# Optimization experiments

Measured on AMD Instinct MI355X. Metric: run time of the kernel, lower is better.

Reference implementation:

```python
import jax, jax.numpy as jnp
import numpy as np

N = 50000      # nodes
E = 800000     # edges (avg degree 16)
D_IN = 64
H = 128        # capacity
LAT = 64       # latent_dim
LN_EPS = 1e-5


def setup_inputs() -> dict:
    key = jax.random.key(0)
    ks = jax.random.split(key, 16)
    inp = {}
    inp["x"] = jax.random.normal(ks[0], (N, D_IN), dtype=jnp.float32)
    inp["edge_index"] = jax.random.randint(ks[1], (2, E), 0, N)
    dims = [(D_IN, H), (H, H), (H, LAT)]
    ki = 2
    for t in ("m", "v"):  # mu tower / logvar tower
        for i, (di, do) in enumerate(dims):
            s = 1.0 / np.sqrt(di)
            inp[f"{t}Wl{i}"] = jax.random.normal(ks[ki], (do, di), jnp.float32) * s; ki += 1
            inp[f"{t}bl{i}"] = jnp.zeros((do,), jnp.float32)
            inp[f"{t}Wr{i}"] = jax.random.normal(ks[ki], (do, di), jnp.float32) * s; ki += 1
            if i < 2:  # LayerNorm on hidden layers only
                inp[f"{t}g{i}"] = jnp.ones((do,), jnp.float32)
                inp[f"{t}b{i}"] = jnp.zeros((do,), jnp.float32)
    return inp


def _ln(h, g, b):
    m = h.mean(-1, keepdims=True)
    v = h.var(-1, keepdims=True)
    return (h - m) * jax.lax.rsqrt(v + LN_EPS) * g + b


def _sage(h, src, dst, inv_deg, Wl, bl, Wr):
    # mean neighbor aggregation: scatter-add messages h[src] into dst, divide by degree
    agg = jax.ops.segment_sum(h[src], dst, num_segments=N) * inv_deg  # [N, d_in]
    # PyG SAGEConv: lin_l(agg) [with bias] + lin_r(h_root) [no bias]
    return agg @ Wl.T + bl + h @ Wr.T


def _tower(x, src, dst, inv_deg, layers):
    h = x
    L = len(layers)
    for i, lay in enumerate(layers):
        h = _sage(h, src, dst, inv_deg, lay[0], lay[1], lay[2])
        if i < L - 1:
            h = jax.nn.relu(_ln(h, lay[3], lay[4]))
    return h


def reference(x, edge_index,
              mWl0, mbl0, mWr0, mg0, mb0,
              mWl1, mbl1, mWr1, mg1, mb1,
              mWl2, mbl2, mWr2,
              vWl0, vbl0, vWr0, vg0, vb0,
              vWl1, vbl1, vWr1, vg1, vb1,
              vWl2, vbl2, vWr2):
    src, dst = edge_index[0], edge_index[1]
    deg = jax.ops.segment_sum(jnp.ones((E,), x.dtype), dst, num_segments=N)
    inv_deg = (1.0 / jnp.maximum(deg, 1.0))[:, None]
    mu_layers = [(mWl0, mbl0, mWr0, mg0, mb0),
                 (mWl1, mbl1, mWr1, mg1, mb1),
                 (mWl2, mbl2, mWr2)]
    lv_layers = [(vWl0, vbl0, vWr0, vg0, vb0),
                 (vWl1, vbl1, vWr1, vg1, vb1),
                 (vWl2, vbl2, vWr2)]
    mu = _tower(x, src, dst, inv_deg, mu_layers)
    lv = _tower(x, src, dst, inv_deg, lv_layers)
    return mu, lv
```

## Files before the change

### kernel.cpp

```cpp
#include <hip/hip_runtime.h>

#define NN 50000
#define NE 800000
#define MPAD 50048
#define NBK 196
#define FB 98
#define CH4 2048
#define EB4 200000
#define STAGE_CAP 6144

typedef __attribute__((ext_vector_type(8))) short short8;
typedef __attribute__((ext_vector_type(4))) float f32x4;
typedef uint __attribute__((ext_vector_type(4))) uintx4;
typedef uint __attribute__((ext_vector_type(2))) uintx2;

__device__ __forceinline__ ushort f2b(float f) {
    uint u = __builtin_bit_cast(uint, f);
    uint r = (u + 0x7fffu + ((u >> 16) & 1u)) >> 16;
    return (ushort)r;
}
__device__ __forceinline__ uint pk2(float a, float b) {
    return (uint)f2b(a) | ((uint)f2b(b) << 16);
}
__device__ __forceinline__ float blo(uint u) { return __builtin_bit_cast(float, u << 16); }
__device__ __forceinline__ float bhi(uint u) { return __builtin_bit_cast(float, u & 0xffff0000u); }

__device__ __forceinline__ uint enc8u(float y) {
    uint b = __builtin_bit_cast(uint, y * 0x1p-120f) + (1u << 19);
    return (b >> 20) & 0x7fu;
}
__device__ __forceinline__ uint enc8s(float y) {
    uint sb = __builtin_bit_cast(uint, y) & 0x80000000u;
    uint b = __builtin_bit_cast(uint, fabsf(y) * 0x1p-120f) + (1u << 19);
    return ((b >> 20) & 0x7fu) | (sb >> 24);
}

__device__ __forceinline__ void acc8(float* a, uintx4 u) {
    a[0] += blo(u[0]); a[1] += bhi(u[0]);
    a[2] += blo(u[1]); a[3] += bhi(u[1]);
    a[4] += blo(u[2]); a[5] += bhi(u[2]);
    a[6] += blo(u[3]); a[7] += bhi(u[3]);
}
__device__ __forceinline__ void acc4(float* a, uintx2 u) {
    a[0] += blo(u[0]); a[1] += bhi(u[0]);
    a[2] += blo(u[1]); a[3] += bhi(u[1]);
}
template <bool SIGNED>
__device__ __forceinline__ void accf8(float* a, uintx2 u, float c120) {
#pragma unroll
    for (int w = 0; w < 2; ++w) {
        uint v = u[w];
#pragma unroll
        for (int j = 0; j < 4; ++j) {
            uint b = (v >> (8 * j)) & 0xffu;
            uint f = SIGNED ? (((b & 0x80u) << 24) | ((b & 0x7fu) << 20)) : (b << 20);
            a[w * 4 + j] += __builtin_bit_cast(float, f) * c120;
        }
    }
}


struct W2Args {
    const float* srcA[8];
    const float* srcB[8];
    ushort* dst[8];
};


struct PrepArgs {
    const float* x; ushort* xb;
    W2Args w;
    const int* edst; int* bhist;
};

__global__ __launch_bounds__(256) void k_prep(PrepArgs a) {
    __shared__ int h[NBK];
    int b = blockIdx.x;
    int t = threadIdx.x;
    if (b < FB) {
        for (int i = t; i < NBK; i += 256) h[i] = 0;
        __syncthreads();
        int i1 = min((b + 1) * CH4, EB4);
        for (int i = b * CH4 + t; i < i1; i += 256) {
            int4 d = ((const int4*)a.edst)[i];
            atomicAdd(&h[d.x >> 8], 1);
            atomicAdd(&h[d.y >> 8], 1);
            atomicAdd(&h[d.z >> 8], 1);
            atomicAdd(&h[d.w >> 8], 1);
        }
        __syncthreads();
        for (int i = t; i < NBK; i += 256) a.bhist[b * NBK + i] = h[i];
    } else if (b < FB + 512) {
        const int offT[8]   = {0, 16384, 49152, 57344, 65536, 81920, 114688, 122880};
        const int splitT[8] = {64, 128, 128, 0, 64, 128, 128, 0};
        const int logKKT[8] = {7, 8, 7, 7, 7, 8, 7, 7};
        const int ntT[8]    = {8, 8, 4, 4, 8, 8, 4, 4};
        int idx = (b - FB) * 256 + t;
        if (idx >= 131072) return;
        int L = 0;
#pragma unroll
        for (int i = 1; i < 8; ++i) if (idx >= offT[i]) L = i;
        int j = idx - offT[L];
        int lk = logKKT[L];
        int KK = 1 << lk;
        int n = j >> lk;
        int c = j & (KK - 1);
        int split = splitT[L];
        float v = (c < split) ? a.w.srcA[L][n * split + c]
                              : a.w.srcB[L][n * (KK - split) + (c - split)];
        int ks = c >> 5, kseg = (c >> 3) & 3, jj = c & 7;
        int nt = n >> 4, r15 = n & 15;
        int lane = (kseg << 4) | r15;
        int foff = ((ks * ntT[L] + nt) << 9) + (lane << 3) + jj;
        a.w.dst[L][foff] = f2b(v);
    } else {
        int i = (b - FB - 512) * 256 + t;
        if (i < NN * 32) {
            float2 v = *(const float2*)(a.x + (size_t)i * 2);
            *(uint*)(a.xb + (size_t)i * 2) = pk2(v.x, v.y);
        }
    }
}


__global__ __launch_bounds__(256) void k_fscan(const int* __restrict__ bhist,
                                               int* __restrict__ pairRel,
                                               int* __restrict__ bbase) {
    __shared__ int tot[256];
    int b = threadIdx.x;
    int run = 0;
    if (b < NBK) {
        for (int blk = 0; blk < FB; ++blk) {
            int v = bhist[blk * NBK + b];
            pairRel[blk * NBK + b] = run;
            run += v;
        }
    }
    tot[b] = (b < NBK) ? run : 0;
    __syncthreads();
    for (int off = 1; off < 256; off <<= 1) {
        int t = (b >= off) ? tot[b - off] : 0;
        __syncthreads();
        tot[b] += t;
        __syncthreads();
    }
    if (b < NBK) bbase[b] = tot[b] - run;
    if (b == NBK - 1) bbase[NBK] = tot[b];
}

__global__ __launch_bounds__(256) void k_f2(const int* __restrict__ src, const int* __restrict__ dst,
                                            const int* __restrict__ pairRel,
                                            const int* __restrict__ bbase, int2* __restrict__ pairs) {
    __shared__ int cur[NBK];
    for (int i = threadIdx.x; i < NBK; i += 256)
        cur[i] = bbase[i] + pairRel[blockIdx.x * NBK + i];
    __syncthreads();
    int i1 = min((int)(blockIdx.x + 1) * CH4, EB4);
    for (int i = blockIdx.x * CH4 + threadIdx.x; i < i1; i += 256) {
        int4 s = ((const int4*)src)[i];
        int4 d = ((const int4*)dst)[i];
        int p0 = atomicAdd(&cur[d.x >> 8], 1);
        int p1 = atomicAdd(&cur[d.y >> 8], 1);
        int p2 = atomicAdd(&cur[d.z >> 8], 1);
        int p3 = atomicAdd(&cur[d.w >> 8], 1);
        pairs[p0] = (int2){s.x, d.x};
        pairs[p1] = (int2){s.y, d.y};
        pairs[p2] = (int2){s.z, d.z};
        pairs[p3] = (int2){s.w, d.w};
    }
}

__global__ __launch_bounds__(256) void k_f3(const int2* __restrict__ pairs,
                                            const int* __restrict__ bbase,
                                            int* __restrict__ row_start,
                                            float* __restrict__ inv_deg,
                                            int* __restrict__ col) {
    __shared__ int ndeg[256];
    __shared__ int noff[256];
    __shared__ int stage[STAGE_CAP];
    int b = blockIdx.x;
    int base = bbase[b], end = bbase[b + 1];
    int nbase = b << 8;
    int t = threadIdx.x;
    ndeg[t] = 0;
    __syncthreads();
    for (int p = base + t; p < end; p += 256) atomicAdd(&ndeg[pairs[p].y - nbase], 1);
    __syncthreads();
    int d = ndeg[t];
    noff[t] = d;
    __syncthreads();
    for (int off = 1; off < 256; off <<= 1) {
        int v = (t >= off) ? noff[t - off] : 0;
        __syncthreads();
        noff[t] += v;
        __syncthreads();
    }
    int excl = noff[t] - d;
    int node = nbase + t;
    if (node < NN) {
        row_start[node] = base + excl;
        inv_deg[node] = 1.0f / (float)(d > 1 ? d : 1);
    }
    if (b == 0 && t == 0) row_start[NN] = NE;
    __syncthreads();
    noff[t] = excl;
    __syncthreads();
    int cnt = end - base;
    for (int p = base + t; p < end; p += 256) {
        int2 pr = pairs[p];
        int pos = atomicAdd(&noff[pr.y - nbase], 1);
        if (pos < STAGE_CAP) stage[pos] = pr.x;
        else col[base + pos] = pr.x;
    }
    __syncthreads();
    int lim = cnt < STAGE_CAP ? cnt : STAGE_CAP;
    for (int i = t; i < lim; i += 256) col[base + i] = stage[i];
}


__global__ __launch_bounds__(256) void k_agg64(
    const ushort* __restrict__ h,
    const int* __restrict__ row_start, const int* __restrict__ col,
    const float* __restrict__ inv_deg, ushort* __restrict__ o) {
    int gid = blockIdx.x * 256 + threadIdx.x;
    int node = gid >> 4;
    int li = gid & 15;
    if (node >= NN) return;
    int s = row_start[node], e = row_start[node + 1];
    float sc = inv_deg[node];
    const ushort* hb = h + li * 4;
    float a[4] = {0, 0, 0, 0};
    int p = s;
    for (; p + 7 < e; p += 8) {
        int cc[8];
#pragma unroll
        for (int j = 0; j < 8; ++j) cc[j] = __builtin_nontemporal_load(col + p + j);
#pragma unroll
        for (int j = 0; j < 8; ++j) acc4(a, *(const uintx2*)(hb + (size_t)cc[j] * 64));
    }
    for (; p < e; ++p) acc4(a, *(const uintx2*)(hb + (size_t)col[p] * 64));
    uintx2 r;
    r[0] = pk2(a[0] * sc, a[1] * sc);
    r[1] = pk2(a[2] * sc, a[3] * sc);
    *(uintx2*)(o + (size_t)node * 64 + li * 4) = r;
}


template <int D, bool SIGNED>
__global__ __launch_bounds__(256) void k_agg8(
    const uchar* __restrict__ h,
    const int* __restrict__ row_start, const int* __restrict__ col,
    const float* __restrict__ inv_deg, ushort* __restrict__ o) {
    constexpr int LPN = D / 8;
    int gid = blockIdx.x * 256 + threadIdx.x;
    int node = gid / LPN;
    int li = gid & (LPN - 1);
    if (node >= NN) return;
    int s = row_start[node], e = row_start[node + 1];
    float sc = inv_deg[node];
    const uchar* hb = h + li * 8;
    const float c120 = 0x1p120f;
    float a[8] = {0, 0, 0, 0, 0, 0, 0, 0};
    int p = s;
    for (; p + 7 < e; p += 8) {
        int cc[8];
#pragma unroll
        for (int j = 0; j < 8; ++j) cc[j] = __builtin_nontemporal_load(col + p + j);
#pragma unroll
        for (int j = 0; j < 8; ++j) accf8<SIGNED>(a, *(const uintx2*)(hb + (size_t)cc[j] * D), c120);
    }
    for (; p < e; ++p) accf8<SIGNED>(a, *(const uintx2*)(hb + (size_t)col[p] * D), c120);
    uintx4 r;
    r[0] = pk2(a[0] * sc, a[1] * sc);
    r[1] = pk2(a[2] * sc, a[3] * sc);
    r[2] = pk2(a[4] * sc, a[5] * sc);
    r[3] = pk2(a[6] * sc, a[7] * sc);
    *(uintx4*)(o + (size_t)node * D + li * 8) = r;
}


struct GArgs {
    const ushort *A1, *A2, *Wm, *Wv;
    const float *blm, *blv, *gm, *gv, *bbm, *bbv;
    void* out;
    uchar* out8;
};

template <int KH, int NOUT, bool DO_LN, bool DUAL, int ASTR, int AOFFM, int OSTR, int OOFFM, bool F8OUT>
__global__ __launch_bounds__(256, 2) void k_gemm(GArgs a) {
    constexpr int NT = NOUT / 16;
    constexpr int NK = KH / 16;
    constexpr int TW = DUAL ? 2 : 1;
    constexpr int WCH = NOUT * KH * 4 / 16;
    __shared__ uint4 wlds[TW * WCH];

    int tid = threadIdx.x;
    int lane = tid & 63, wid = tid >> 6;
    int tow = DUAL ? 0 : blockIdx.y;
    int aoff = tow * AOFFM;

    {
        const uint4* w0 = (const uint4*)(tow ? a.Wv : a.Wm);
        for (int i = tid; i < WCH; i += 256) wlds[i] = w0[i];
        if (DUAL) {
            const uint4* w1 = (const uint4*)a.Wv;
            for (int i = tid; i < WCH; i += 256) wlds[WCH + i] = w1[i];
        }
    }

    int r15 = lane & 15, kseg = lane >> 4;
    int m0 = blockIdx.x * 128 + wid * 32;
    size_t ar0 = (size_t)(m0 + r15);
    size_t ar1 = (size_t)(m0 + 16 + r15);

    short8 af[2][NK];
#pragma unroll
    for (int ks = 0; ks < NK; ++ks) {
        int kc = ks * 32 + kseg * 8;
        af[0][ks] = (kc < KH) ? *(const short8*)(a.A1 + ar0 * ASTR + aoff + kc)
                              : *(const short8*)(a.A2 + ar0 * ASTR + aoff + (kc - KH));
        af[1][ks] = (kc < KH) ? *(const short8*)(a.A1 + ar1 * ASTR + aoff + kc)
                              : *(const short8*)(a.A2 + ar1 * ASTR + aoff + (kc - KH));
    }
    __syncthreads();

    f32x4 acc[TW][2][NT];
#pragma unroll
    for (int tt = 0; tt < TW; ++tt)
#pragma unroll
        for (int t = 0; t < 2; ++t)
#pragma unroll
            for (int nt = 0; nt < NT; ++nt) acc[tt][t][nt] = (f32x4){0.f, 0.f, 0.f, 0.f};

#pragma unroll
    for (int ks = 0; ks < NK; ++ks) {
#pragma unroll
        for (int nt = 0; nt < NT; ++nt) {
#pragma unroll
            for (int tt = 0; tt < TW; ++tt) {
                short8 w = *(const short8*)&wlds[tt * WCH + (ks * NT + nt) * 64 + lane];
                acc[tt][0][nt] = __builtin_amdgcn_mfma_f32_16x16x32_bf16(af[0][ks], w, acc[tt][0][nt], 0, 0, 0);
                acc[tt][1][nt] = __builtin_amdgcn_mfma_f32_16x16x32_bf16(af[1][ks], w, acc[tt][1][nt], 0, 0, 0);
            }
        }
    }

#pragma unroll
    for (int tt = 0; tt < TW; ++tt) {
        int tsel = DUAL ? tt : tow;
        int ooff = tsel * OOFFM;
        const float* bl = tsel ? a.blv : a.blm;
#pragma unroll
        for (int nt = 0; nt < NT; ++nt) {
            float bb = bl[nt * 16 + r15];
#pragma unroll
            for (int t = 0; t < 2; ++t)
#pragma unroll
                for (int r = 0; r < 4; ++r) acc[tt][t][nt][r] += bb;
        }
        if (DO_LN) {
            const float* g = tsel ? a.gv : a.gm;
            const float* b = tsel ? a.bbv : a.bbm;
#pragma unroll
            for (int t = 0; t < 2; ++t) {
                float s[4] = {0, 0, 0, 0}, q[4] = {0, 0, 0, 0};
#pragma unroll
                for (int nt = 0; nt < NT; ++nt)
#pragma unroll
                    for (int r = 0; r < 4; ++r) { float v = acc[tt][t][nt][r]; s[r] += v; q[r] += v * v; }
#pragma unroll
                for (int off = 1; off < 16; off <<= 1)
#pragma unroll
                    for (int r = 0; r < 4; ++r) { s[r] += __shfl_xor(s[r], off); q[r] += __shfl_xor(q[r], off); }
                float mean[4], rstd[4];
#pragma unroll
                for (int r = 0; r < 4; ++r) {
                    mean[r] = s[r] * (1.0f / NOUT);
                    float var = q[r] * (1.0f / NOUT) - mean[r] * mean[r];
                    rstd[r] = rsqrtf(var + 1e-5f);
                }
                ushort* out = (ushort*)a.out;
#pragma unroll
                for (int nt = 0; nt < NT; ++nt) {
                    int n = nt * 16 + r15;
                    float gg = g[n], bb = b[n];
#pragma unroll
                    for (int r = 0; r < 4; ++r) {
                        int row = m0 + t * 16 + kseg * 4 + r;
                        if (row < NN) {
                            float y = fmaxf((acc[tt][t][nt][r] - mean[r]) * rstd[r] * gg + bb, 0.0f);
                            out[(size_t)row * OSTR + ooff + n] = f2b(y);
                            if (F8OUT) a.out8[(size_t)row * OSTR + ooff + n] = (uchar)enc8u(y);
                        }
                    }
                }
            }
        } else {
            float* out = (float*)a.out;
#pragma unroll
            for (int t = 0; t < 2; ++t)
#pragma unroll
                for (int nt = 0; nt < NT; ++nt) {
                    int n = nt * 16 + r15;
#pragma unroll
                    for (int r = 0; r < 4; ++r) {
                        int row = m0 + t * 16 + kseg * 4 + r;
                        if (row < NN) out[(size_t)row * OSTR + ooff + n] = acc[tt][t][nt][r];
                    }
                }
        }
    }
}


struct G2Args {
    const ushort *A, *Wm, *Wv, *a2;
    const float *blm, *blv;
    void *outm, *outv;
};

template <bool FINAL>
__global__ __launch_bounds__(256, 2) void k_gemm2(G2Args a) {
    constexpr int NT = 4, NK = 4;
    constexpr int WCH = 1024;
    __shared__ uint4 wlds[WCH];

    int tid = threadIdx.x;
    int lane = tid & 63, wid = tid >> 6;
    int tow = blockIdx.y;
    {
        const uint4* w0 = (const uint4*)(tow ? a.Wv : a.Wm);
        for (int i = tid; i < WCH; i += 256) wlds[i] = w0[i];
    }
    int r15 = lane & 15, kseg = lane >> 4;
    int m0 = blockIdx.x * 128 + wid * 32;
    size_t ar0 = (size_t)(m0 + r15);
    size_t ar1 = (size_t)(m0 + 16 + r15);
    int aoff = tow * 128;

    short8 af[2][NK];
#pragma unroll
    for (int ks = 0; ks < NK; ++ks) {
        int kc = ks * 32 + kseg * 8;
        af[0][ks] = *(const short8*)(a.A + ar0 * 256 + aoff + kc);
        af[1][ks] = *(const short8*)(a.A + ar1 * 256 + aoff + kc);
    }
    __syncthreads();

    f32x4 acc[2][NT];
#pragma unroll
    for (int t = 0; t < 2; ++t)
#pragma unroll
        for (int nt = 0; nt < NT; ++nt) acc[t][nt] = (f32x4){0.f, 0.f, 0.f, 0.f};

#pragma unroll
    for (int ks = 0; ks < NK; ++ks) {
#pragma unroll
        for (int nt = 0; nt < NT; ++nt) {
            short8 w = *(const short8*)&wlds[(ks * NT + nt) * 64 + lane];
            acc[0][nt] = __builtin_amdgcn_mfma_f32_16x16x32_bf16(af[0][ks], w, acc[0][nt], 0, 0, 0);
            acc[1][nt] = __builtin_amdgcn_mfma_f32_16x16x32_bf16(af[1][ks], w, acc[1][nt], 0, 0, 0);
        }
    }

    if (FINAL) {
        const float* bl = tow ? a.blv : a.blm;
        float* out = (float*)(tow ? a.outv : a.outm);
#pragma unroll
        for (int t = 0; t < 2; ++t)
#pragma unroll
            for (int nt = 0; nt < NT; ++nt) {
                int n = nt * 16 + r15;
                float bb = bl[n];
#pragma unroll
                for (int r = 0; r < 4; ++r) {
                    int row = m0 + t * 16 + kseg * 4 + r;
                    if (row < NN) {
                        float av = blo((uint)a.a2[(size_t)row * 128 + tow * 64 + n]);
                        out[(size_t)row * 64 + n] = acc[t][nt][r] + bb + av;
                    }
                }
            }
    } else {
        uchar* out = (uchar*)a.outm;
#pragma unroll
        for (int t = 0; t < 2; ++t)
#pragma unroll
            for (int nt = 0; nt < NT; ++nt) {
                int n = nt * 16 + r15;
#pragma unroll
                for (int r = 0; r < 4; ++r) {
                    int row = m0 + t * 16 + kseg * 4 + r;
                    if (row < NN) out[(size_t)row * 128 + tow * 64 + n] = (uchar)enc8s(acc[t][nt][r]);
                }
            }
    }
}


extern "C" void kernel_launch(void* const* d_in, const int* in_sizes, int n_in,
                              void* d_out, int out_size, void* d_ws, size_t ws_size,
                              hipStream_t stream) {
    const float* x = (const float*)d_in[0];
    const int* ei = (const int*)d_in[1];
    const int* esrc = ei;
    const int* edst = ei + NE;

    const float* mWl0 = (const float*)d_in[2];
    const float* mbl0 = (const float*)d_in[3];
    const float* mWr0 = (const float*)d_in[4];
    const float* mg0  = (const float*)d_in[5];
    const float* mb0  = (const float*)d_in[6];
    const float* mWl1 = (const float*)d_in[7];
    const float* mbl1 = (const float*)d_in[8];
    const float* mWr1 = (const float*)d_in[9];
    const float* mg1  = (const float*)d_in[10];
    const float* mb1  = (const float*)d_in[11];
    const float* mWl2 = (const float*)d_in[12];
    const float* mbl2 = (const float*)d_in[13];
    const float* mWr2 = (const float*)d_in[14];
    const float* vWl0 = (const float*)d_in[15];
    const float* vbl0 = (const float*)d_in[16];
    const float* vWr0 = (const float*)d_in[17];
    const float* vg0  = (const float*)d_in[18];
    const float* vb0  = (const float*)d_in[19];
    const float* vWl1 = (const float*)d_in[20];
    const float* vbl1 = (const float*)d_in[21];
    const float* vWr1 = (const float*)d_in[22];
    const float* vg1  = (const float*)d_in[23];
    const float* vb1  = (const float*)d_in[24];
    const float* vWl2 = (const float*)d_in[25];
    const float* vbl2 = (const float*)d_in[26];
    const float* vWr2 = (const float*)d_in[27];

    char* p = (char*)d_ws;
    auto alloc = [&](size_t bytes) {
        void* r = (void*)p;
        p += (bytes + 255) & ~(size_t)255;
        return r;
    };
    int* bhist     = (int*)alloc((size_t)FB * NBK * 4);
    int* pairRel   = (int*)alloc((size_t)FB * NBK * 4);
    int* bbase     = (int*)alloc((size_t)(NBK + 1) * 4);
    int* row_start = (int*)alloc((size_t)(NN + 1) * 4);
    float* inv_deg = (float*)alloc((size_t)NN * 4);
    int* col       = (int*)alloc((size_t)NE * 4);
    int2* pairs    = (int2*)alloc((size_t)NE * 8);
    ushort* agg0   = (ushort*)pairs;
    ushort* x_bf   = (ushort*)alloc((size_t)MPAD * 64 * 2);
    ushort* h1p    = (ushort*)alloc((size_t)MPAD * 256 * 2);
    ushort* h2p    = (ushort*)alloc((size_t)MPAD * 256 * 2);
    ushort* aggp   = (ushort*)alloc((size_t)MPAD * 256 * 2);
    uchar* h1f8    = (uchar*)h2p;
    uchar* p2f8    = (uchar*)aggp;
    ushort* a2     = aggp + (size_t)MPAD * 128;
    ushort* wc0    = (ushort*)alloc((size_t)128 * 128 * 2);
    ushort* wc1    = (ushort*)alloc((size_t)128 * 256 * 2);
    ushort* wc2    = (ushort*)alloc((size_t)64 * 128 * 2);
    ushort* wc3    = (ushort*)alloc((size_t)128 * 128 * 2);
    ushort* wc4    = (ushort*)alloc((size_t)128 * 256 * 2);
    ushort* wc5    = (ushort*)alloc((size_t)64 * 128 * 2);
    ushort* wc6    = (ushort*)alloc((size_t)64 * 128 * 2);
    ushort* wc7    = (ushort*)alloc((size_t)64 * 128 * 2);

    float* out_mu = (float*)d_out;
    float* out_lv = (float*)d_out + (size_t)NN * 64;

    PrepArgs pa;
    pa.x = x; pa.xb = x_bf; pa.edst = edst; pa.bhist = bhist;
    pa.w.srcA[0] = mWl0; pa.w.srcB[0] = mWr0; pa.w.dst[0] = wc0;
    pa.w.srcA[1] = mWl1; pa.w.srcB[1] = mWr1; pa.w.dst[1] = wc1;
    pa.w.srcA[2] = mWl2; pa.w.srcB[2] = nullptr; pa.w.dst[2] = wc2;
    pa.w.srcA[3] = nullptr; pa.w.srcB[3] = mWr2; pa.w.dst[3] = wc6;
    pa.w.srcA[4] = vWl0; pa.w.srcB[4] = vWr0; pa.w.dst[4] = wc3;
    pa.w.srcA[5] = vWl1; pa.w.srcB[5] = vWr1; pa.w.dst[5] = wc4;
    pa.w.srcA[6] = vWl2; pa.w.srcB[6] = nullptr; pa.w.dst[6] = wc5;
    pa.w.srcA[7] = nullptr; pa.w.srcB[7] = vWr2; pa.w.dst[7] = wc7;
    k_prep<<<FB + 512 + (NN * 32 + 255) / 256, 256, 0, stream>>>(pa);

    k_fscan<<<1, 256, 0, stream>>>(bhist, pairRel, bbase);
    k_f2<<<FB, 256, 0, stream>>>(esrc, edst, pairRel, bbase, pairs);
    k_f3<<<NBK, 256, 0, stream>>>(pairs, bbase, row_start, inv_deg, col);

    const int gM = MPAD / 128;

    k_agg64<<<(NN * 16 + 255) / 256, 256, 0, stream>>>(x_bf, row_start, col, inv_deg, agg0);
    {
        GArgs ga = {agg0, x_bf, wc0, wc3, mbl0, vbl0, mg0, vg0, mb0, vb0, h1p, h1f8};
        k_gemm<64, 128, true, true, 64, 0, 256, 128, true><<<dim3(gM, 1), 256, 0, stream>>>(ga);
    }
    k_agg8<256, false><<<(NN * 32 + 255) / 256, 256, 0, stream>>>(h1f8, row_start, col, inv_deg, aggp);
    {
        GArgs ga = {aggp, h1p, wc1, wc4, mbl1, vbl1, mg1, vg1, mb1, vb1, h2p, nullptr};
        k_gemm<128, 128, true, false, 256, 128, 256, 128, false><<<dim3(gM, 2), 256, 0, stream>>>(ga);
    }
    {
        G2Args g2 = {h2p, wc2, wc5, nullptr, nullptr, nullptr, p2f8, nullptr};
        k_gemm2<false><<<dim3(gM, 2), 256, 0, stream>>>(g2);
    }
    k_agg8<128, true><<<(NN * 16 + 255) / 256, 256, 0, stream>>>(p2f8, row_start, col, inv_deg, a2);
    {
        G2Args g2 = {h2p, wc6, wc7, a2, mbl2, vbl2, out_mu, out_lv};
        k_gemm2<true><<<dim3(gM, 2), 256, 0, stream>>>(g2);
    }
}
```

Before: 352.6 us.

## Double-buffer weight staging in k_gemm and make row tile configurable

```diff
diff --git a/kernel.cpp b/kernel.cpp
--- a/kernel.cpp
+++ b/kernel.cpp
@@ -35,12 +35,6 @@
     return ((b >> 20) & 0x7fu) | (sb >> 24);
 }
 
-__device__ __forceinline__ void acc8(float* a, uintx4 u) {
-    a[0] += blo(u[0]); a[1] += bhi(u[0]);
-    a[2] += blo(u[1]); a[3] += bhi(u[1]);
-    a[4] += blo(u[2]); a[5] += bhi(u[2]);
-    a[6] += blo(u[3]); a[7] += bhi(u[3]);
-}
 __device__ __forceinline__ void acc4(float* a, uintx2 u) {
     a[0] += blo(u[0]); a[1] += bhi(u[0]);
     a[2] += blo(u[1]); a[3] += bhi(u[1]);
@@ -286,63 +280,83 @@
     uchar* out8;
 };
 
-template <int KH, int NOUT, bool DO_LN, bool DUAL, int ASTR, int AOFFM, int OSTR, int OOFFM, bool F8OUT>
-__global__ __launch_bounds__(256, 2) void k_gemm(GArgs a) {
+template <int KH, int NOUT, bool DO_LN, bool DUAL, int ASTR, int AOFFM, int OSTR, int OOFFM, bool F8OUT, int RT>
+__global__ __launch_bounds__(256, 3) void k_gemm(GArgs a) {
     constexpr int NT = NOUT / 16;
     constexpr int NK = KH / 16;
     constexpr int TW = DUAL ? 2 : 1;
-    constexpr int WCH = NOUT * KH * 4 / 16;
-    __shared__ uint4 wlds[TW * WCH];
+    constexpr int KSB = (TW * NT >= 16) ? 1 : (16 / (TW * NT));
+    constexpr int NC = NK / KSB;
+    constexpr int TCH = KSB * NT * 64;
+    constexpr int CPT = TW * TCH;
+    __shared__ uint4 wlds[2][CPT];
 
     int tid = threadIdx.x;
     int lane = tid & 63, wid = tid >> 6;
     int tow = DUAL ? 0 : blockIdx.y;
     int aoff = tow * AOFFM;
-
-    {
-        const uint4* w0 = (const uint4*)(tow ? a.Wv : a.Wm);
-        for (int i = tid; i < WCH; i += 256) wlds[i] = w0[i];
+    const uint4* w0g = (const uint4*)(tow ? a.Wv : a.Wm);
+    const uint4* w1g = (const uint4*)a.Wv;
+
+    int r15 = lane & 15, kseg = lane >> 4;
+    int m0 = blockIdx.x * (64 * RT) + wid * (16 * RT);
+    size_t ar[RT];
+#pragma unroll
+    for (int t = 0; t < RT; ++t) ar[t] = (size_t)(m0 + t * 16 + r15);
+
+    short8 af[2][RT][KSB];
+
+    auto stageW = [&](int c, int b) {
+        const uint4* p0 = w0g + (size_t)c * TCH;
+#pragma unroll
+        for (int i = 0; i < TCH / 256; ++i) wlds[b][i * 256 + tid] = p0[i * 256 + tid];
         if (DUAL) {
-            const uint4* w1 = (const uint4*)a.Wv;
-            for (int i = tid; i < WCH; i += 256) wlds[WCH + i] = w1[i];
-        }
-    }
-
-    int r15 = lane & 15, kseg = lane >> 4;
-    int m0 = blockIdx.x * 128 + wid * 32;
-    size_t ar0 = (size_t)(m0 + r15);
-    size_t ar1 = (size_t)(m0 + 16 + r15);
-
-    short8 af[2][NK];
-#pragma unroll
-    for (int ks = 0; ks < NK; ++ks) {
-        int kc = ks * 32 + kseg * 8;
-        af[0][ks] = (kc < KH) ? *(const short8*)(a.A1 + ar0 * ASTR + aoff + kc)
-                              : *(const short8*)(a.A2 + ar0 * ASTR + aoff + (kc - KH));
-        af[1][ks] = (kc < KH) ? *(const short8*)(a.A1 + ar1 * ASTR + aoff + kc)
-                              : *(const short8*)(a.A2 + ar1 * ASTR + aoff + (kc - KH));
-    }
-    __syncthreads();
-
-    f32x4 acc[TW][2][NT];
+            const uint4* p1 = w1g + (size_t)c * TCH;
+#pragma unroll
+            for (int i = 0; i < TCH / 256; ++i) wlds[b][TCH + i * 256 + tid] = p1[i * 256 + tid];
+        }
+    };
+    auto loadA = [&](int c, int b) {
+#pragma unroll
+        for (int ko = 0; ko < KSB; ++ko) {
+            int kc = (c * KSB + ko) * 32 + kseg * 8;
+#pragma unroll
+            for (int t = 0; t < RT; ++t)
+                af[b][t][ko] = (kc < KH) ? *(const short8*)(a.A1 + ar[t] * ASTR + aoff + kc)
+                                         : *(const short8*)(a.A2 + ar[t] * ASTR + aoff + (kc - KH));
+        }
+    };
+
+    loadA(0, 0);
+    stageW(0, 0);
+    __syncthreads();
+
+    f32x4 acc[TW][RT][NT];
 #pragma unroll
     for (int tt = 0; tt < TW; ++tt)
 #pragma unroll
-        for (int t = 0; t < 2; ++t)
+        for (int t = 0; t < RT; ++t)
 #pragma unroll
             for (int nt = 0; nt < NT; ++nt) acc[tt][t][nt] = (f32x4){0.f, 0.f, 0.f, 0.f};
 
 #pragma unroll
-    for (int ks = 0; ks < NK; ++ks) {
-#pragma unroll
-        for (int nt = 0; nt < NT; ++nt) {
-#pragma unroll
-            for (int tt = 0; tt < TW; ++tt) {
-                short8 w = *(const short8*)&wlds[tt * WCH + (ks * NT + nt) * 64 + lane];
-                acc[tt][0][nt] = __builtin_amdgcn_mfma_f32_16x16x32_bf16(af[0][ks], w, acc[tt][0][nt], 0, 0, 0);
-                acc[tt][1][nt] = __builtin_amdgcn_mfma_f32_16x16x32_bf16(af[1][ks], w, acc[tt][1][nt], 0, 0, 0);
+    for (int c = 0; c < NC; ++c) {
+        int b = c & 1;
+        if (c + 1 < NC) { stageW(c + 1, b ^ 1); loadA(c + 1, b ^ 1); }
+#pragma unroll
+        for (int ko = 0; ko < KSB; ++ko) {
+#pragma unroll
+            for (int nt = 0; nt < NT; ++nt) {
+#pragma unroll
+                for (int tt = 0; tt < TW; ++tt) {
+                    short8 w = *(const short8*)&wlds[b][tt * TCH + (ko * NT + nt) * 64 + lane];
+#pragma unroll
+                    for (int t = 0; t < RT; ++t)
+                        acc[tt][t][nt] = __builtin_amdgcn_mfma_f32_16x16x32_bf16(af[b][t][ko], w, acc[tt][t][nt], 0, 0, 0);
+                }
             }
         }
+        __syncthreads();
     }
 
 #pragma unroll
@@ -354,15 +368,15 @@
         for (int nt = 0; nt < NT; ++nt) {
             float bb = bl[nt * 16 + r15];
 #pragma unroll
-            for (int t = 0; t < 2; ++t)
+            for (int t = 0; t < RT; ++t)
 #pragma unroll
                 for (int r = 0; r < 4; ++r) acc[tt][t][nt][r] += bb;
         }
         if (DO_LN) {
             const float* g = tsel ? a.gv : a.gm;
-            const float* b = tsel ? a.bbv : a.bbm;
-#pragma unroll
-            for (int t = 0; t < 2; ++t) {
+            const float* b2 = tsel ? a.bbv : a.bbm;
+#pragma unroll
+            for (int t = 0; t < RT; ++t) {
                 float s[4] = {0, 0, 0, 0}, q[4] = {0, 0, 0, 0};
 #pragma unroll
                 for (int nt = 0; nt < NT; ++nt)
@@ -383,7 +397,7 @@
 #pragma unroll
                 for (int nt = 0; nt < NT; ++nt) {
                     int n = nt * 16 + r15;
-                    float gg = g[n], bb = b[n];
+                    float gg = g[n], bb = b2[n];
 #pragma unroll
                     for (int r = 0; r < 4; ++r) {
                         int row = m0 + t * 16 + kseg * 4 + r;
@@ -398,7 +412,7 @@
         } else {
             float* out = (float*)a.out;
 #pragma unroll
-            for (int t = 0; t < 2; ++t)
+            for (int t = 0; t < RT; ++t)
 #pragma unroll
                 for (int nt = 0; nt < NT; ++nt) {
                     int n = nt * 16 + r15;
@@ -582,25 +596,23 @@
     k_f2<<<FB, 256, 0, stream>>>(esrc, edst, pairRel, bbase, pairs);
     k_f3<<<NBK, 256, 0, stream>>>(pairs, bbase, row_start, inv_deg, col);
 
-    const int gM = MPAD / 128;
-
     k_agg64<<<(NN * 16 + 255) / 256, 256, 0, stream>>>(x_bf, row_start, col, inv_deg, agg0);
     {
         GArgs ga = {agg0, x_bf, wc0, wc3, mbl0, vbl0, mg0, vg0, mb0, vb0, h1p, h1f8};
-        k_gemm<64, 128, true, true, 64, 0, 256, 128, true><<<dim3(gM, 1), 256, 0, stream>>>(ga);
+        k_gemm<64, 128, true, true, 64, 0, 256, 128, true, 1><<<dim3(MPAD / 64, 1), 256, 0, stream>>>(ga);
     }
     k_agg8<256, false><<<(NN * 32 + 255) / 256, 256, 0, stream>>>(h1f8, row_start, col, inv_deg, aggp);
     {
         GArgs ga = {aggp, h1p, wc1, wc4, mbl1, vbl1, mg1, vg1, mb1, vb1, h2p, nullptr};
-        k_gemm<128, 128, true, false, 256, 128, 256, 128, false><<<dim3(gM, 2), 256, 0, stream>>>(ga);
+        k_gemm<128, 128, true, false, 256, 128, 256, 128, false, 2><<<dim3(MPAD / 128, 2), 256, 0, stream>>>(ga);
     }
     {
         G2Args g2 = {h2p, wc2, wc5, nullptr, nullptr, nullptr, p2f8, nullptr};
-        k_gemm2<false><<<dim3(gM, 2), 256, 0, stream>>>(g2);
+        k_gemm2<false><<<dim3(MPAD / 128, 2), 256, 0, stream>>>(g2);
     }
     k_agg8<128, true><<<(NN * 16 + 255) / 256, 256, 0, stream>>>(p2f8, row_start, col, inv_deg, a2);
     {
         G2Args g2 = {h2p, wc6, wc7, a2, mbl2, vbl2, out_mu, out_lv};
-        k_gemm2<true><<<dim3(gM, 2), 256, 0, stream>>>(g2);
-    }
-}
+        k_gemm2<true><<<dim3(MPAD / 128, 2), 256, 0, stream>>>(g2);
+    }
+}
```

Result: faster. 329.3 us (-6.6%).
